# Kernel optimization log

Hardware: AMD Instinct MI355X
Metric: run time of the kernel (lower is better)

Reference implementation:

```python
import jax, jax.numpy as jnp
import numpy as np

VOCAB = 32000
EMB = 512
HID = 1024
SEQ = 512
BATCH = 128


def setup_inputs() -> dict:
    key = jax.random.key(0)
    ks = jax.random.split(key, 12)
    s = 0.02
    return {
        "x": jax.random.randint(ks[0], (BATCH,), 0, VOCAB, dtype=jnp.int32),
        "encoder_states": jax.random.normal(ks[1], (SEQ, BATCH, 2 * HID), jnp.float32),
        "hidden": jax.random.normal(ks[2], (1, BATCH, HID), jnp.float32),
        "cell": jax.random.normal(ks[3], (1, BATCH, HID), jnp.float32),
        "emb_table": jax.random.normal(ks[4], (VOCAB, EMB), jnp.float32) * s,
        "W_e": jax.random.normal(ks[5], (3 * HID, 1), jnp.float32) * s,
        "b_e": jnp.zeros((1,), jnp.float32),
        "W_ih": jax.random.normal(ks[6], (4 * HID, 2 * HID + EMB), jnp.float32) * s,
        "W_hh": jax.random.normal(ks[7], (4 * HID, HID), jnp.float32) * s,
        "b_ih": jnp.zeros((4 * HID,), jnp.float32),
        "b_hh": jnp.zeros((4 * HID,), jnp.float32),
        "W_fc": jax.random.normal(ks[8], (VOCAB, HID), jnp.float32) * s,
        "b_fc": jnp.zeros((VOCAB,), jnp.float32),
    }


def reference(x, encoder_states, hidden, cell, emb_table, W_e, b_e,
              W_ih, W_hh, b_ih, b_hh, W_fc, b_fc):
    # x: [B] token ids (single decode step). Dropout = eval-mode identity.
    emb = emb_table[x]  # [B, E]
    S = encoder_states.shape[0]
    # hidden.repeat(S,1,1): [1,B,H] -> [S,B,H]
    h_rep = jnp.broadcast_to(hidden, (S,) + hidden.shape[1:])
    # energy: relu(Linear(cat(h, enc_states)))  -> [S, B, 1]
    energy = jax.nn.relu(jnp.concatenate([h_rep, encoder_states], axis=-1) @ W_e + b_e)
    # softmax over the sequence dim (dim=0)
    attn = jax.nn.softmax(energy[..., 0], axis=0)  # [S, B]
    # bmm(attention [B,1,S], enc [B,S,2H]) -> context [B, 2H]
    context = jnp.einsum('sb,sbh->bh', attn, encoder_states)
    # single-step LSTM on cat(context, embedding)
    rnn_in = jnp.concatenate([context, emb], axis=-1)  # [B, 2H+E]
    gates = rnn_in @ W_ih.T + b_ih + hidden[0] @ W_hh.T + b_hh  # [B, 4H]
    i_g, f_g, g_g, o_g = jnp.split(gates, 4, axis=-1)  # torch gate order i,f,g,o
    i_g = jax.nn.sigmoid(i_g)
    f_g = jax.nn.sigmoid(f_g)
    g_g = jnp.tanh(g_g)
    o_g = jax.nn.sigmoid(o_g)
    c_new = f_g * cell[0] + i_g * g_g
    h_new = o_g * jnp.tanh(c_new)
    predictions = h_new @ W_fc.T + b_fc  # [B, VOCAB]
    return predictions, h_new[None], c_new[None]
```

## Files before the change

### kernel.cpp

```cpp
#include <hip/hip_runtime.h>
#include <cstdint>
#include <cstddef>

#define VOCAB 32000
#define EMB 512
#define HID 1024
#define SEQ 512
#define BATCH 128
#define SPLIT 8

typedef __bf16 bf16x8 __attribute__((ext_vector_type(8)));
typedef short  s16x8  __attribute__((ext_vector_type(8)));
typedef float  f32x4  __attribute__((ext_vector_type(4)));

__device__ __forceinline__ float sigmoidf_(float x) { return 1.f / (1.f + __expf(-x)); }

__device__ __forceinline__ unsigned short f2bu(float f) {
    union { float f; uint32_t u; } v; v.f = f;
    return (unsigned short)((v.u + 0x7FFFu + ((v.u >> 16) & 1u)) >> 16);
}

__device__ __forceinline__ bf16x8 cvt_bf8(float4 a, float4 b) {
    union { s16x8 s; bf16x8 b; } u;
    u.s[0] = (short)f2bu(a.x); u.s[1] = (short)f2bu(a.y);
    u.s[2] = (short)f2bu(a.z); u.s[3] = (short)f2bu(a.w);
    u.s[4] = (short)f2bu(b.x); u.s[5] = (short)f2bu(b.y);
    u.s[6] = (short)f2bu(b.z); u.s[7] = (short)f2bu(b.w);
    return u.b;
}

__device__ __forceinline__ bf16x8 load_bf8(const unsigned short* p) {
    union { s16x8 s; bf16x8 b; } u;
    u.s = *(const s16x8*)p;
    return u.b;
}

__global__ void init_k(float* __restrict__ gates, unsigned short* __restrict__ hid_bf,
                       const float* __restrict__ b_ih, const float* __restrict__ b_hh,
                       const float* __restrict__ hidden)
{
    const int i = blockIdx.x * 256 + threadIdx.x;
    const int ng = BATCH * 4 * HID;
    if (i < ng) {
        const int r = i & (4 * HID - 1);
        gates[i] = b_ih[r] + b_hh[r];
    } else {
        const int j = i - ng;
        if (j < BATCH * HID) hid_bf[j] = f2bu(hidden[j]);
    }
}

__global__ __launch_bounds__(256, 4) void attn_k(
    const float* __restrict__ enc, const float* __restrict__ hidden,
    const float* __restrict__ W_e, const float* __restrict__ b_e,
    float* __restrict__ ctxPartial, float* __restrict__ lPartial)
{
    const int blk  = blockIdx.x;
    const int b    = blk >> 3;
    const int chnk = blk & 7;
    const int t    = threadIdx.x;
    const int wave = t >> 6;
    const int lane = t & 63;

    __shared__ float red[4];
    __shared__ float l_sh[4];
    __shared__ float ctx_sh[4][2048];

    float4 hv = *(const float4*)&hidden[(size_t)b * HID + t * 4];
    float4 wv = *(const float4*)&W_e[t * 4];
    float hl = hv.x * wv.x + hv.y * wv.y + hv.z * wv.z + hv.w * wv.w;
    #pragma unroll
    for (int off = 32; off > 0; off >>= 1) hl += __shfl_down(hl, off, 64);
    if (lane == 0) red[wave] = hl;
    __syncthreads();
    const float hdot = red[0] + red[1] + red[2] + red[3] + b_e[0];

    float4 w[8];
    #pragma unroll
    for (int j = 0; j < 8; j++)
        w[j] = *(const float4*)&W_e[HID + j * 256 + lane * 4];

    float4 c[8];
    #pragma unroll
    for (int j = 0; j < 8; j++) c[j] = make_float4(0.f, 0.f, 0.f, 0.f);
    float lsum = 0.f;

    #pragma unroll 1
    for (int i = 0; i < 16; i++) {
        const int s = chnk * 64 + wave + i * 4;
        const float* p = enc + ((size_t)s * BATCH + b) * 2048;
        float4 e[8];
        #pragma unroll
        for (int j = 0; j < 8; j++)
            e[j] = *(const float4*)&p[j * 256 + lane * 4];
        float d = 0.f;
        #pragma unroll
        for (int j = 0; j < 8; j++)
            d += e[j].x * w[j].x + e[j].y * w[j].y + e[j].z * w[j].z + e[j].w * w[j].w;
        #pragma unroll
        for (int off = 32; off > 0; off >>= 1) d += __shfl_xor(d, off, 64);
        float energy = d + hdot;
        energy = energy > 0.f ? energy : 0.f;
        const float pr = __expf(energy);
        lsum += pr;
        #pragma unroll
        for (int j = 0; j < 8; j++) {
            c[j].x += pr * e[j].x; c[j].y += pr * e[j].y;
            c[j].z += pr * e[j].z; c[j].w += pr * e[j].w;
        }
    }

    #pragma unroll
    for (int j = 0; j < 8; j++)
        *(float4*)&ctx_sh[wave][j * 256 + lane * 4] = c[j];
    if (lane == 0) l_sh[wave] = lsum;
    __syncthreads();

    float* outp = ctxPartial + (size_t)blk * 2048;
    #pragma unroll
    for (int j = 0; j < 8; j++) {
        const int idx = j * 256 + t;
        outp[idx] = ctx_sh[0][idx] + ctx_sh[1][idx] + ctx_sh[2][idx] + ctx_sh[3][idx];
    }
    if (t == 0) lPartial[blk] = l_sh[0] + l_sh[1] + l_sh[2] + l_sh[3];
}

__global__ void combine_k(const float* __restrict__ ctxPartial,
                          const float* __restrict__ lPartial,
                          const int* __restrict__ x,
                          const float* __restrict__ emb_table,
                          unsigned short* __restrict__ rnn_bf)
{
    const int b = blockIdx.x;
    const int t = threadIdx.x;
    float L = 0.f;
    #pragma unroll
    for (int cN = 0; cN < SPLIT; cN++) L += lPartial[b * SPLIT + cN];
    const float inv = 1.f / L;
    unsigned short* out = rnn_bf + (size_t)b * 2560;
    #pragma unroll
    for (int j = 0; j < 8; j++) {
        const int h = j * 256 + t;
        float v = 0.f;
        #pragma unroll
        for (int cN = 0; cN < SPLIT; cN++)
            v += ctxPartial[((size_t)(b * SPLIT + cN)) * 2048 + h];
        out[h] = f2bu(v * inv);
    }
    const int tok = x[b];
    for (int e2 = t; e2 < EMB; e2 += 256)
        out[2048 + e2] = f2bu(emb_table[(size_t)tok * EMB + e2]);
}

__global__ __launch_bounds__(256) void gates_mfma_k(
    float* __restrict__ gates,
    const unsigned short* __restrict__ rnn_bf, const unsigned short* __restrict__ hid_bf,
    const float* __restrict__ W_ih, const float* __restrict__ W_hh)
{
    const int chunk = blockIdx.y;
    const unsigned short* X; const float* W; int Kx, Kw;
    if (chunk < 5) { X = rnn_bf + chunk * 512; W = W_ih + chunk * 512; Kx = 2560; Kw = 2560; }
    else           { X = hid_bf + (chunk - 5) * 512; W = W_hh + (chunk - 5) * 512; Kx = 1024; Kw = 1024; }

    const int t    = threadIdx.x;
    const int wave = t >> 6;
    const int lane = t & 63;
    const int ln   = lane & 15;
    const int q    = lane >> 4;
    const int n0   = (blockIdx.x * 4 + wave) * 16;

    f32x4 acc[8];
    #pragma unroll
    for (int mt = 0; mt < 8; mt++) acc[mt] = (f32x4){0.f, 0.f, 0.f, 0.f};

    const float* wrow = W + (size_t)(n0 + ln) * Kw;

    #pragma unroll 2
    for (int kk = 0; kk < 512; kk += 32) {
        const int k = kk + q * 8;
        float4 b0 = *(const float4*)&wrow[k];
        float4 b1 = *(const float4*)&wrow[k + 4];
        bf16x8 bf = cvt_bf8(b0, b1);
        #pragma unroll
        for (int mt = 0; mt < 8; mt++) {
            bf16x8 af = load_bf8(&X[(size_t)(mt * 16 + ln) * Kx + k]);
            acc[mt] = __builtin_amdgcn_mfma_f32_16x16x32_bf16(af, bf, acc[mt], 0, 0, 0);
        }
    }

    #pragma unroll
    for (int mt = 0; mt < 8; mt++) {
        #pragma unroll
        for (int r = 0; r < 4; r++) {
            const int m = mt * 16 + q * 4 + r;
            atomicAdd(&gates[(size_t)m * (4 * HID) + n0 + ln], acc[mt][r]);
        }
    }
}

__global__ void lstm_k(const float* __restrict__ gates, const float* __restrict__ cell,
                       float* __restrict__ h_out, float* __restrict__ c_out,
                       unsigned short* __restrict__ h_bf)
{
    const int idx = blockIdx.x * 256 + threadIdx.x;
    const int b = idx >> 10;
    const int h = idx & 1023;
    const float* g = gates + (size_t)b * (4 * HID);
    const float ig = sigmoidf_(g[h]);
    const float fg = sigmoidf_(g[HID + h]);
    const float gg = tanhf(g[2 * HID + h]);
    const float og = sigmoidf_(g[3 * HID + h]);
    const float cn = fg * cell[idx] + ig * gg;
    const float hn = og * tanhf(cn);
    c_out[idx] = cn;
    h_out[idx] = hn;
    h_bf[idx] = f2bu(hn);
}

__global__ __launch_bounds__(256) void fc_mfma_k(
    float* __restrict__ pred, const unsigned short* __restrict__ h_bf,
    const float* __restrict__ W_fc, const float* __restrict__ b_fc)
{
    const int t    = threadIdx.x;
    const int wave = t >> 6;
    const int lane = t & 63;
    const int ln   = lane & 15;
    const int q    = lane >> 4;
    const int n0   = (blockIdx.x * 4 + wave) * 16;

    f32x4 acc[8];
    #pragma unroll
    for (int mt = 0; mt < 8; mt++) acc[mt] = (f32x4){0.f, 0.f, 0.f, 0.f};

    const float* wrow = W_fc + (size_t)(n0 + ln) * HID;

    #pragma unroll 2
    for (int kk = 0; kk < HID; kk += 32) {
        const int k = kk + q * 8;
        float4 b0 = *(const float4*)&wrow[k];
        float4 b1 = *(const float4*)&wrow[k + 4];
        bf16x8 bf = cvt_bf8(b0, b1);
        #pragma unroll
        for (int mt = 0; mt < 8; mt++) {
            bf16x8 af = load_bf8(&h_bf[(size_t)(mt * 16 + ln) * HID + k]);
            acc[mt] = __builtin_amdgcn_mfma_f32_16x16x32_bf16(af, bf, acc[mt], 0, 0, 0);
        }
    }

    const float bias = b_fc[n0 + ln];
    #pragma unroll
    for (int mt = 0; mt < 8; mt++) {
        #pragma unroll
        for (int r = 0; r < 4; r++) {
            const int m = mt * 16 + q * 4 + r;
            pred[(size_t)m * VOCAB + n0 + ln] = acc[mt][r] + bias;
        }
    }
}

extern "C" void kernel_launch(void* const* d_in, const int* in_sizes, int n_in,
                              void* d_out, int out_size, void* d_ws, size_t ws_size,
                              hipStream_t stream)
{
    const int*   x      = (const int*)  d_in[0];
    const float* enc    = (const float*)d_in[1];
    const float* hidden = (const float*)d_in[2];
    const float* cell   = (const float*)d_in[3];
    const float* emb    = (const float*)d_in[4];
    const float* W_e    = (const float*)d_in[5];
    const float* b_e    = (const float*)d_in[6];
    const float* W_ih   = (const float*)d_in[7];
    const float* W_hh   = (const float*)d_in[8];
    const float* b_ih   = (const float*)d_in[9];
    const float* b_hh   = (const float*)d_in[10];
    const float* W_fc   = (const float*)d_in[11];
    const float* b_fc   = (const float*)d_in[12];

    float* pred  = (float*)d_out;
    float* h_out = pred + (size_t)BATCH * VOCAB;
    float* c_out = h_out + BATCH * HID;

    float* ws         = (float*)d_ws;
    float* ctxPartial = ws;
    float* lPartial   = ctxPartial + (size_t)BATCH * SPLIT * 2048;
    float* gates      = lPartial + BATCH * SPLIT;
    unsigned short* rnn_bf = (unsigned short*)(gates + (size_t)BATCH * 4 * HID);
    unsigned short* hid_bf = rnn_bf + (size_t)BATCH * 2560;
    unsigned short* h_bf   = hid_bf + (size_t)BATCH * HID;

    init_k<<<2560, 256, 0, stream>>>(gates, hid_bf, b_ih, b_hh, hidden);
    attn_k<<<BATCH * SPLIT, 256, 0, stream>>>(enc, hidden, W_e, b_e, ctxPartial, lPartial);
    combine_k<<<BATCH, 256, 0, stream>>>(ctxPartial, lPartial, x, emb, rnn_bf);
    gates_mfma_k<<<dim3(64, 7), 256, 0, stream>>>(gates, rnn_bf, hid_bf, W_ih, W_hh);
    lstm_k<<<(BATCH * HID) / 256, 256, 0, stream>>>(gates, cell, h_out, c_out, h_bf);
    fc_mfma_k<<<VOCAB / 64, 256, 0, stream>>>(pred, h_bf, W_fc, b_fc);
}
```

Before: 957.0 us.

## Replace gate atomics with per-chunk partials, fold init into attn and lstm, add nontemporal loads

Removes the init kernel: the hidden-to-bf16 conversion moves into attn_k (chunk 0 blocks) and the bias sum moves into lstm_k. The gates GEMM now writes per-K-chunk partial sums to a 7-slice workspace instead of doing float atomicAdds, and lstm_k reduces the 7 partials. Streaming reads of encoder states and weight matrices use nontemporal loads to avoid polluting cache. This saves one launch and atomic contention, at the cost of extra workspace traffic (7x gate buffer write/read).

```diff
diff --git a/kernel.cpp b/kernel.cpp
--- a/kernel.cpp
+++ b/kernel.cpp
@@ -8,10 +8,12 @@
 #define SEQ 512
 #define BATCH 128
 #define SPLIT 8
+#define NCHUNK 7
 
 typedef __bf16 bf16x8 __attribute__((ext_vector_type(8)));
 typedef short  s16x8  __attribute__((ext_vector_type(8)));
 typedef float  f32x4  __attribute__((ext_vector_type(4)));
+typedef float  fvec4  __attribute__((ext_vector_type(4)));
 
 __device__ __forceinline__ float sigmoidf_(float x) { return 1.f / (1.f + __expf(-x)); }
 
@@ -35,25 +37,16 @@
     return u.b;
 }
 
-__global__ void init_k(float* __restrict__ gates, unsigned short* __restrict__ hid_bf,
-                       const float* __restrict__ b_ih, const float* __restrict__ b_hh,
-                       const float* __restrict__ hidden)
-{
-    const int i = blockIdx.x * 256 + threadIdx.x;
-    const int ng = BATCH * 4 * HID;
-    if (i < ng) {
-        const int r = i & (4 * HID - 1);
-        gates[i] = b_ih[r] + b_hh[r];
-    } else {
-        const int j = i - ng;
-        if (j < BATCH * HID) hid_bf[j] = f2bu(hidden[j]);
-    }
+__device__ __forceinline__ float4 ldnt4(const float* p) {
+    fvec4 v = __builtin_nontemporal_load((const fvec4*)p);
+    return make_float4(v.x, v.y, v.z, v.w);
 }
 
 __global__ __launch_bounds__(256, 4) void attn_k(
     const float* __restrict__ enc, const float* __restrict__ hidden,
     const float* __restrict__ W_e, const float* __restrict__ b_e,
-    float* __restrict__ ctxPartial, float* __restrict__ lPartial)
+    float* __restrict__ ctxPartial, float* __restrict__ lPartial,
+    unsigned short* __restrict__ hid_bf)
 {
     const int blk  = blockIdx.x;
     const int b    = blk >> 3;
@@ -67,6 +60,10 @@
     __shared__ float ctx_sh[4][2048];
 
     float4 hv = *(const float4*)&hidden[(size_t)b * HID + t * 4];
+    if (chnk == 0) {
+        unsigned short hb[4] = { f2bu(hv.x), f2bu(hv.y), f2bu(hv.z), f2bu(hv.w) };
+        *(uint2*)&hid_bf[(size_t)b * HID + t * 4] = *(const uint2*)hb;
+    }
     float4 wv = *(const float4*)&W_e[t * 4];
     float hl = hv.x * wv.x + hv.y * wv.y + hv.z * wv.z + hv.w * wv.w;
     #pragma unroll
@@ -92,7 +89,7 @@
         float4 e[8];
         #pragma unroll
         for (int j = 0; j < 8; j++)
-            e[j] = *(const float4*)&p[j * 256 + lane * 4];
+            e[j] = ldnt4(&p[j * 256 + lane * 4]);
         float d = 0.f;
         #pragma unroll
         for (int j = 0; j < 8; j++)
@@ -153,7 +150,7 @@
 }
 
 __global__ __launch_bounds__(256) void gates_mfma_k(
-    float* __restrict__ gates,
+    float* __restrict__ gP,
     const unsigned short* __restrict__ rnn_bf, const unsigned short* __restrict__ hid_bf,
     const float* __restrict__ W_ih, const float* __restrict__ W_hh)
 {
@@ -178,8 +175,8 @@
     #pragma unroll 2
     for (int kk = 0; kk < 512; kk += 32) {
         const int k = kk + q * 8;
-        float4 b0 = *(const float4*)&wrow[k];
-        float4 b1 = *(const float4*)&wrow[k + 4];
+        float4 b0 = ldnt4(&wrow[k]);
+        float4 b1 = ldnt4(&wrow[k + 4]);
         bf16x8 bf = cvt_bf8(b0, b1);
         #pragma unroll
         for (int mt = 0; mt < 8; mt++) {
@@ -188,28 +185,43 @@
         }
     }
 
+    float* outp = gP + (size_t)chunk * (BATCH * 4 * HID);
     #pragma unroll
     for (int mt = 0; mt < 8; mt++) {
         #pragma unroll
         for (int r = 0; r < 4; r++) {
             const int m = mt * 16 + q * 4 + r;
-            atomicAdd(&gates[(size_t)m * (4 * HID) + n0 + ln], acc[mt][r]);
-        }
-    }
-}
-
-__global__ void lstm_k(const float* __restrict__ gates, const float* __restrict__ cell,
+            outp[(size_t)m * (4 * HID) + n0 + ln] = acc[mt][r];
+        }
+    }
+}
+
+__global__ void lstm_k(const float* __restrict__ gP,
+                       const float* __restrict__ b_ih, const float* __restrict__ b_hh,
+                       const float* __restrict__ cell,
                        float* __restrict__ h_out, float* __restrict__ c_out,
                        unsigned short* __restrict__ h_bf)
 {
     const int idx = blockIdx.x * 256 + threadIdx.x;
     const int b = idx >> 10;
     const int h = idx & 1023;
-    const float* g = gates + (size_t)b * (4 * HID);
-    const float ig = sigmoidf_(g[h]);
-    const float fg = sigmoidf_(g[HID + h]);
-    const float gg = tanhf(g[2 * HID + h]);
-    const float og = sigmoidf_(g[3 * HID + h]);
+    float g0 = b_ih[h]            + b_hh[h];
+    float g1 = b_ih[HID + h]      + b_hh[HID + h];
+    float g2 = b_ih[2 * HID + h]  + b_hh[2 * HID + h];
+    float g3 = b_ih[3 * HID + h]  + b_hh[3 * HID + h];
+    const float* base = gP + (size_t)b * (4 * HID);
+    #pragma unroll
+    for (int cN = 0; cN < NCHUNK; cN++) {
+        const float* p = base + (size_t)cN * (BATCH * 4 * HID);
+        g0 += p[h];
+        g1 += p[HID + h];
+        g2 += p[2 * HID + h];
+        g3 += p[3 * HID + h];
+    }
+    const float ig = sigmoidf_(g0);
+    const float fg = sigmoidf_(g1);
+    const float gg = tanhf(g2);
+    const float og = sigmoidf_(g3);
     const float cn = fg * cell[idx] + ig * gg;
     const float hn = og * tanhf(cn);
     c_out[idx] = cn;
@@ -237,8 +249,8 @@
     #pragma unroll 2
     for (int kk = 0; kk < HID; kk += 32) {
         const int k = kk + q * 8;
-        float4 b0 = *(const float4*)&wrow[k];
-        float4 b1 = *(const float4*)&wrow[k + 4];
+        float4 b0 = ldnt4(&wrow[k]);
+        float4 b1 = ldnt4(&wrow[k + 4]);
         bf16x8 bf = cvt_bf8(b0, b1);
         #pragma unroll
         for (int mt = 0; mt < 8; mt++) {
@@ -283,15 +295,16 @@
     float* ws         = (float*)d_ws;
     float* ctxPartial = ws;
     float* lPartial   = ctxPartial + (size_t)BATCH * SPLIT * 2048;
-    float* gates      = lPartial + BATCH * SPLIT;
-    unsigned short* rnn_bf = (unsigned short*)(gates + (size_t)BATCH * 4 * HID);
+    float* gP         = lPartial + BATCH * SPLIT;
+    unsigned short* rnn_bf = (unsigned short*)(gP + (size_t)NCHUNK * BATCH * 4 * HID);
     unsigned short* hid_bf = rnn_bf + (size_t)BATCH * 2560;
     unsigned short* h_bf   = hid_bf + (size_t)BATCH * HID;
 
-    init_k<<<2560, 256, 0, stream>>>(gates, hid_bf, b_ih, b_hh, hidden);
-    attn_k<<<BATCH * SPLIT, 256, 0, stream>>>(enc, hidden, W_e, b_e, ctxPartial, lPartial);
+    attn_k<<<BATCH * SPLIT, 256, 0, stream>>>(enc, hidden, W_e, b_e,
+                                              ctxPartial, lPartial, hid_bf);
     combine_k<<<BATCH, 256, 0, stream>>>(ctxPartial, lPartial, x, emb, rnn_bf);
-    gates_mfma_k<<<dim3(64, 7), 256, 0, stream>>>(gates, rnn_bf, hid_bf, W_ih, W_hh);
-    lstm_k<<<(BATCH * HID) / 256, 256, 0, stream>>>(gates, cell, h_out, c_out, h_bf);
+    gates_mfma_k<<<dim3(64, NCHUNK), 256, 0, stream>>>(gP, rnn_bf, hid_bf, W_ih, W_hh);
+    lstm_k<<<(BATCH * HID) / 256, 256, 0, stream>>>(gP, b_ih, b_hh, cell,
+                                                    h_out, c_out, h_bf);
     fc_mfma_k<<<VOCAB / 64, 256, 0, stream>>>(pred, h_bf, W_fc, b_fc);
 }
```

New measurement: 919.5 us. -3.9%, faster.
